# Optimization experiments

Hardware: AMD Instinct MI355X
Metric: run time of the kernel (lower is better)

Reference implementation:

```python
import jax, jax.numpy as jnp
import numpy as np

B, C, H, Wd = 4, 64, 64, 64


def setup_inputs() -> dict:
    key = jax.random.key(0)
    k1, k2, k3 = jax.random.split(key, 3)
    x = jax.random.normal(k1, (B, C, H, Wd), dtype=jnp.float32)
    W = jax.random.normal(k2, (C, C), dtype=jnp.float32) * (1.0 / np.sqrt(C))
    b = jax.random.normal(k3, (C,), dtype=jnp.float32) * 0.01
    return {"x": x, "W": W, "b": b}


def reference(x, W, b):
    Bz, Cz, Hz, Wz = x.shape
    N = Hz * Wz
    xf = x.reshape(Bz, Cz, N)                      # values [B,C,N]
    # shared 1x1 conv for queries and keys (same module instance in torch)
    qk = jnp.einsum('oc,bcn->bon', W, xf) + b[None, :, None]  # [B,C,N]
    # scores[b,n,m] = sum_c q[b,c,n] * k[b,c,m], scaled by 1/N
    scores = jnp.einsum('bcn,bcm->bnm', qk, qk) / N           # [B,N,N]
    attn = jax.nn.softmax(scores, axis=-1)                    # softmax over m
    # out[b,c,n] = sum_m values[b,c,m] * attn[b,n,m]
    out = jnp.einsum('bcm,bnm->bcn', xf, attn)
    return out.reshape(Bz, Cz, Hz, Wz)
```

## Files before the change

### kernel.cpp

```cpp
#include <hip/hip_runtime.h>
#include <hip/hip_bf16.h>

#define BATCH 4
#define NSP   4096

#define QKSCALE 0.0187675376f

typedef __bf16 bf16x8v __attribute__((ext_vector_type(8)));
typedef __bf16 bf16x4v __attribute__((ext_vector_type(4)));
typedef float  floatx4 __attribute__((ext_vector_type(4)));
typedef float  floatx16 __attribute__((ext_vector_type(16)));
typedef unsigned uivec2 __attribute__((ext_vector_type(2)));

static __device__ __forceinline__ float fast_exp2(float x) {
#if __has_builtin(__builtin_amdgcn_exp2f)
    return __builtin_amdgcn_exp2f(x);
#else
    return exp2f(x);
#endif
}

static __device__ __forceinline__ unsigned pkbf(float a, float b) {
    union { __bf16 h[2]; unsigned u; } x;
    x.h[0] = (__bf16)a; x.h[1] = (__bf16)b;
    return x.u;
}

static __device__ __forceinline__ void plswap(unsigned &a, unsigned &b) {
#if __has_builtin(__builtin_amdgcn_permlane32_swap)
    uivec2 r = __builtin_amdgcn_permlane32_swap(a, b, false, false);
    a = r[0]; b = r[1];
#else
    asm("v_permlane32_swap_b32 %0, %1" : "+v"(a), "+v"(b));
#endif
}

__global__ __launch_bounds__(256) void qk_kernel(const float* __restrict__ x,
                                                 const float* __restrict__ Wm,
                                                 const float* __restrict__ bias,
                                                 __bf16* __restrict__ qkT,
                                                 __bf16* __restrict__ xbf) {
    __shared__ __align__(16) __bf16 xT[64 * 72];

    const int t  = threadIdx.x;
    const int b  = blockIdx.x >> 6;
    const int n0 = (blockIdx.x & 63) << 6;

#pragma unroll
    for (int p = 0; p < 4; ++p) {
        const int c  = p * 16 + (t >> 4);
        const int n4 = (t & 15) * 4;
        const float4 v = *(const float4*)(x + (size_t)(b * 64 + c) * 4096 + n0 + n4);
        xT[(n4 + 0) * 72 + c] = (__bf16)(v.x * QKSCALE);
        xT[(n4 + 1) * 72 + c] = (__bf16)(v.y * QKSCALE);
        xT[(n4 + 2) * 72 + c] = (__bf16)(v.z * QKSCALE);
        xT[(n4 + 3) * 72 + c] = (__bf16)(v.w * QKSCALE);
        bf16x4v xv;
        xv[0] = (__bf16)v.x; xv[1] = (__bf16)v.y; xv[2] = (__bf16)v.z; xv[3] = (__bf16)v.w;
        *(bf16x4v*)(xbf + (size_t)(b * 64 + c) * 4096 + n0 + n4) = xv;
    }
    __syncthreads();

    const int w = t >> 6, lane = t & 63, quad = lane >> 4, l16 = lane & 15;
    const bf16x8v a0 = *(const bf16x8v*)(xT + (w * 16 + l16) * 72 + quad * 8);
    const bf16x8v a1 = *(const bf16x8v*)(xT + (w * 16 + l16) * 72 + 32 + quad * 8);

    floatx4 acc[4];
#pragma unroll
    for (int ot = 0; ot < 4; ++ot) {
        const float* wr = Wm + (ot * 16 + l16) * 64;
        float4 wa = *(const float4*)(wr + quad * 8);
        float4 wb = *(const float4*)(wr + quad * 8 + 4);
        float4 wc = *(const float4*)(wr + 32 + quad * 8);
        float4 wd = *(const float4*)(wr + 32 + quad * 8 + 4);
        bf16x8v b0, b1;
        b0[0]=(__bf16)wa.x; b0[1]=(__bf16)wa.y; b0[2]=(__bf16)wa.z; b0[3]=(__bf16)wa.w;
        b0[4]=(__bf16)wb.x; b0[5]=(__bf16)wb.y; b0[6]=(__bf16)wb.z; b0[7]=(__bf16)wb.w;
        b1[0]=(__bf16)wc.x; b1[1]=(__bf16)wc.y; b1[2]=(__bf16)wc.z; b1[3]=(__bf16)wc.w;
        b1[4]=(__bf16)wd.x; b1[5]=(__bf16)wd.y; b1[6]=(__bf16)wd.z; b1[7]=(__bf16)wd.w;
        acc[ot] = floatx4{0.f, 0.f, 0.f, 0.f};
        acc[ot] = __builtin_amdgcn_mfma_f32_16x16x32_bf16(a0, b0, acc[ot], 0, 0, 0);
        acc[ot] = __builtin_amdgcn_mfma_f32_16x16x32_bf16(a1, b1, acc[ot], 0, 0, 0);
    }
    __syncthreads();

#pragma unroll
    for (int ot = 0; ot < 4; ++ot) {
        const float bo = bias[ot * 16 + l16] * QKSCALE;
#pragma unroll
        for (int r = 0; r < 4; ++r)
            xT[(w * 16 + quad * 4 + r) * 72 + ot * 16 + l16] = (__bf16)(acc[ot][r] + bo);
    }
    __syncthreads();

    const int n = t >> 2, seg = t & 3;
    __bf16* dst = qkT + (size_t)(b * 4096 + n0 + n) * 64 + seg * 16;
    *(bf16x8v*)dst       = *(const bf16x8v*)(xT + n * 72 + seg * 16);
    *(bf16x8v*)(dst + 8) = *(const bf16x8v*)(xT + n * 72 + seg * 16 + 8);
}

template<int SPLIT, int ITERS>
__global__ __launch_bounds__(256, 2) void attn_kernel(const __bf16* __restrict__ xbf,
                                                      const __bf16* __restrict__ qkT,
                                                      __bf16* __restrict__ Opart,
                                                      float* __restrict__ Lpart) {
    __shared__ __align__(16) char smem[66560];
    __bf16* Klds = (__bf16*)smem;
    __bf16* Vlds = (__bf16*)(smem + 16384);
    float*  Olds = (float*)smem;

    const int t   = threadIdx.x;
    const int blk = blockIdx.x;
    const int xcd = blk & 7;
    const int b   = xcd >> 1;
    const int sub = ((blk >> 3) << 1) | (xcd & 1);
    const int qt  = sub / SPLIT;
    const int s   = sub % SPLIT;
    const int n0  = qt << 8;
    const int pblk = (b * 16 + qt) * SPLIT + s;

    const int w = t >> 6, lane = t & 63, l31 = lane & 31, hi = lane >> 5;

    const __bf16* kgl = qkT + (size_t)b * 4096 * 64;
    const __bf16* vgl = xbf + (size_t)b * 64 * 4096;

    bf16x8v qf[2][4];
#pragma unroll
    for (int qt2 = 0; qt2 < 2; ++qt2) {
        const __bf16* qrow = kgl + (size_t)(n0 + w * 64 + qt2 * 32 + l31) * 64;
#pragma unroll
        for (int kb = 0; kb < 4; ++kb)
            qf[qt2][kb] = *(const bf16x8v*)(qrow + kb * 16 + hi * 8);
    }

    floatx16 oacc[2][2] = {};
    float rs[2] = {0.f, 0.f};

    const int srow = t >> 3;
    const int scol = t & 7;
    const int slot = ((scol ^ (srow & 7)) * 8);
    uint4 kst0, kst1, vst0, vst1;
    auto stage_load = [&](int m0) {
        kst0 = *(const uint4*)(kgl + (size_t)(m0 + srow) * 64 + scol * 8);
        kst1 = *(const uint4*)(kgl + (size_t)(m0 + srow + 32) * 64 + scol * 8);
        vst0 = *(const uint4*)(vgl + (size_t)srow * 4096 + m0 + scol * 8);
        vst1 = *(const uint4*)(vgl + (size_t)(srow + 32) * 4096 + m0 + scol * 8);
    };
    auto stage_write = [&](int buf) {
        __bf16* kd = Klds + buf * 4096;
        __bf16* vd = Vlds + buf * 4096;
        *(uint4*)(kd + srow * 64 + slot)        = kst0;
        *(uint4*)(kd + (srow + 32) * 64 + slot) = kst1;
        *(uint4*)(vd + srow * 64 + slot)        = vst0;
        *(uint4*)(vd + (srow + 32) * 64 + slot) = vst1;
    };

    const int mbase = s * (64 * ITERS);
    stage_load(mbase);
    stage_write(0);
    int cur = 0;

    for (int it = 0; it < ITERS; ++it) {
        if (it + 1 < ITERS) stage_load(mbase + ((it + 1) << 6));
        __syncthreads();
        const __bf16* Kc = Klds + cur * 4096;
        const __bf16* Vc = Vlds + cur * 4096;

        __builtin_amdgcn_s_setprio(1);
#pragma unroll
        for (int mt = 0; mt < 2; ++mt) {
            bf16x8v kf[4];
#pragma unroll
            for (int kb = 0; kb < 4; ++kb)
                kf[kb] = *(const bf16x8v*)(Kc + (mt * 32 + l31) * 64 +
                                           (((kb * 2 + hi) ^ (l31 & 7)) * 8));

            bf16x8v vf[2][2];
#pragma unroll
            for (int ct = 0; ct < 2; ++ct)
#pragma unroll
                for (int ks = 0; ks < 2; ++ks)
                    vf[ct][ks] = *(const bf16x8v*)(Vc + (ct * 32 + l31) * 64 +
                                                   (((mt * 4 + ks * 2 + hi) ^ (l31 & 7)) * 8));

#pragma unroll
            for (int qt2 = 0; qt2 < 2; ++qt2) {
                floatx16 acc = {};
#pragma unroll
                for (int kb = 0; kb < 4; ++kb)
                    acc = __builtin_amdgcn_mfma_f32_32x32x16_bf16(kf[kb], qf[qt2][kb], acc, 0, 0, 0);

                float p[16];
                float sum = 0.f;
#pragma unroll
                for (int i = 0; i < 16; ++i) { p[i] = fast_exp2(acc[i]); sum += p[i]; }
                rs[qt2] += sum;

                unsigned wd0 = pkbf(p[0],  p[1]),  wd1 = pkbf(p[2],  p[3]);
                unsigned wd2 = pkbf(p[4],  p[5]),  wd3 = pkbf(p[6],  p[7]);
                unsigned wd4 = pkbf(p[8],  p[9]),  wd5 = pkbf(p[10], p[11]);
                unsigned wd6 = pkbf(p[12], p[13]), wd7 = pkbf(p[14], p[15]);
                plswap(wd0, wd2);
                plswap(wd1, wd3);
                plswap(wd4, wd6);
                plswap(wd5, wd7);
                union { unsigned u[4]; bf16x8v v; } pb0, pb1;
                pb0.u[0] = wd0; pb0.u[1] = wd1; pb0.u[2] = wd2; pb0.u[3] = wd3;
                pb1.u[0] = wd4; pb1.u[1] = wd5; pb1.u[2] = wd6; pb1.u[3] = wd7;

#pragma unroll
                for (int ct = 0; ct < 2; ++ct) {
                    oacc[qt2][ct] = __builtin_amdgcn_mfma_f32_32x32x16_bf16(vf[ct][0], pb0.v, oacc[qt2][ct], 0, 0, 0);
                    oacc[qt2][ct] = __builtin_amdgcn_mfma_f32_32x32x16_bf16(vf[ct][1], pb1.v, oacc[qt2][ct], 0, 0, 0);
                }
            }
        }
        __builtin_amdgcn_s_setprio(0);

        if (it + 1 < ITERS) stage_write(cur ^ 1);
        cur ^= 1;
    }

#pragma unroll
    for (int qt2 = 0; qt2 < 2; ++qt2) {
        float v = rs[qt2] + __shfl_xor(rs[qt2], 32, 64);
        if (lane < 32)
            Lpart[(size_t)pblk * 256 + w * 64 + qt2 * 32 + l31] = v;
    }

    __syncthreads();

#pragma unroll
    for (int qt2 = 0; qt2 < 2; ++qt2)
#pragma unroll
        for (int ct = 0; ct < 2; ++ct)
#pragma unroll
            for (int r = 0; r < 16; ++r) {
                const int c = ct * 32 + (r & 3) + 8 * (r >> 2) + 4 * hi;
                Olds[c * 260 + w * 64 + qt2 * 32 + l31] = oacc[qt2][ct][r];
            }
    __syncthreads();

    const int c = t >> 2, qb = (t & 3) * 64;
#pragma unroll
    for (int i = 0; i < 8; ++i) {
        floatx4 v0 = *(const floatx4*)(Olds + c * 260 + qb + i * 8);
        floatx4 v1 = *(const floatx4*)(Olds + c * 260 + qb + i * 8 + 4);
        bf16x8v pk;
        pk[0]=(__bf16)v0[0]; pk[1]=(__bf16)v0[1]; pk[2]=(__bf16)v0[2]; pk[3]=(__bf16)v0[3];
        pk[4]=(__bf16)v1[0]; pk[5]=(__bf16)v1[1]; pk[6]=(__bf16)v1[2]; pk[7]=(__bf16)v1[3];
        *(bf16x8v*)(Opart + (size_t)pblk * 16384 + c * 256 + qb + i * 8) = pk;
    }
}

template<int SPLIT>
__global__ __launch_bounds__(256) void reduce_kernel(const __bf16* __restrict__ Opart,
                                                     const float* __restrict__ Lpart,
                                                     float* __restrict__ out) {
    const int blk = blockIdx.x;
    const int bq = blk >> 3, cq = blk & 7;
    const int b = bq >> 4, qt = bq & 15;
    const int t = threadIdx.x;
    const int c  = cq * 8 + (t >> 5);
    const int q8 = (t & 31) * 8;

    float l[8] = {0.f,0.f,0.f,0.f,0.f,0.f,0.f,0.f};
#pragma unroll
    for (int s = 0; s < SPLIT; ++s) {
        const float* lp = Lpart + ((size_t)bq * SPLIT + s) * 256 + q8;
        float4 u = *(const float4*)lp;
        float4 v = *(const float4*)(lp + 4);
        l[0]+=u.x; l[1]+=u.y; l[2]+=u.z; l[3]+=u.w;
        l[4]+=v.x; l[5]+=v.y; l[6]+=v.z; l[7]+=v.w;
    }
    float a[8] = {0.f,0.f,0.f,0.f,0.f,0.f,0.f,0.f};
#pragma unroll
    for (int s = 0; s < SPLIT; ++s) {
        bf16x8v v = *(const bf16x8v*)(Opart + ((size_t)bq * SPLIT + s) * 16384 + c * 256 + q8);
#pragma unroll
        for (int k = 0; k < 8; ++k) a[k] += (float)v[k];
    }
    float* op = out + (size_t)(b * 64 + c) * 4096 + qt * 256 + q8;
    float4 o0, o1;
    o0.x = a[0]/l[0]; o0.y = a[1]/l[1]; o0.z = a[2]/l[2]; o0.w = a[3]/l[3];
    o1.x = a[4]/l[4]; o1.y = a[5]/l[5]; o1.z = a[6]/l[6]; o1.w = a[7]/l[7];
    *(float4*)op       = o0;
    *(float4*)(op + 4) = o1;
}

extern "C" void kernel_launch(void* const* d_in, const int* in_sizes, int n_in,
                              void* d_out, int out_size, void* d_ws, size_t ws_size,
                              hipStream_t stream) {
    const float* x    = (const float*)d_in[0];
    const float* Wm   = (const float*)d_in[1];
    const float* bias = (const float*)d_in[2];
    float* out = (float*)d_out;

    char* ws = (char*)d_ws;
    __bf16* qkT = (__bf16*)ws;
    __bf16* xbf = (__bf16*)(ws + 2097152);

    qk_kernel<<<BATCH * (NSP / 64), 256, 0, stream>>>(x, Wm, bias, qkT, xbf);

    const size_t HEAD = 2097152 + 2097152;
    const size_t needBig = HEAD + (size_t)512 * 16384 * 2 + (size_t)512 * 256 * 4;
    if (ws_size >= needBig) {
        __bf16* Opart = (__bf16*)(ws + HEAD);
        float*  Lpart = (float*)(ws + HEAD + (size_t)512 * 16384 * 2);
        attn_kernel<8, 8><<<BATCH * 16 * 8, 256, 0, stream>>>(xbf, qkT, Opart, Lpart);
        reduce_kernel<8><<<512, 256, 0, stream>>>(Opart, Lpart, out);
    } else {
        __bf16* Opart = (__bf16*)(ws + HEAD);
        float*  Lpart = (float*)(ws + HEAD + (size_t)256 * 16384 * 2);
        attn_kernel<4, 16><<<BATCH * 16 * 4, 256, 0, stream>>>(xbf, qkT, Opart, Lpart);
        reduce_kernel<4><<<512, 256, 0, stream>>>(Opart, Lpart, out);
    }
}
```

Baseline: 98.37 us.

## Use 8 waves per attention block with one 32-query tile per wave

Result: faster. 96.33 us (-2.1%).

```diff
diff --git a/kernel.cpp b/kernel.cpp
--- a/kernel.cpp
+++ b/kernel.cpp
@@ -100,7 +100,7 @@
 }
 
 template<int SPLIT, int ITERS>
-__global__ __launch_bounds__(256, 2) void attn_kernel(const __bf16* __restrict__ xbf,
+__global__ __launch_bounds__(512, 4) void attn_kernel(const __bf16* __restrict__ xbf,
                                                       const __bf16* __restrict__ qkT,
                                                       __bf16* __restrict__ Opart,
                                                       float* __restrict__ Lpart) {
@@ -124,35 +124,28 @@
     const __bf16* kgl = qkT + (size_t)b * 4096 * 64;
     const __bf16* vgl = xbf + (size_t)b * 64 * 4096;
 
-    bf16x8v qf[2][4];
-#pragma unroll
-    for (int qt2 = 0; qt2 < 2; ++qt2) {
-        const __bf16* qrow = kgl + (size_t)(n0 + w * 64 + qt2 * 32 + l31) * 64;
+    bf16x8v qf[4];
+    {
+        const __bf16* qrow = kgl + (size_t)(n0 + w * 32 + l31) * 64;
 #pragma unroll
         for (int kb = 0; kb < 4; ++kb)
-            qf[qt2][kb] = *(const bf16x8v*)(qrow + kb * 16 + hi * 8);
-    }
-
-    floatx16 oacc[2][2] = {};
-    float rs[2] = {0.f, 0.f};
+            qf[kb] = *(const bf16x8v*)(qrow + kb * 16 + hi * 8);
+    }
+
+    floatx16 oacc[2] = {};
+    float rs = 0.f;
 
     const int srow = t >> 3;
     const int scol = t & 7;
     const int slot = ((scol ^ (srow & 7)) * 8);
-    uint4 kst0, kst1, vst0, vst1;
+    uint4 kst, vst;
     auto stage_load = [&](int m0) {
-        kst0 = *(const uint4*)(kgl + (size_t)(m0 + srow) * 64 + scol * 8);
-        kst1 = *(const uint4*)(kgl + (size_t)(m0 + srow + 32) * 64 + scol * 8);
-        vst0 = *(const uint4*)(vgl + (size_t)srow * 4096 + m0 + scol * 8);
-        vst1 = *(const uint4*)(vgl + (size_t)(srow + 32) * 4096 + m0 + scol * 8);
+        kst = *(const uint4*)(kgl + (size_t)(m0 + srow) * 64 + scol * 8);
+        vst = *(const uint4*)(vgl + (size_t)srow * 4096 + m0 + scol * 8);
     };
     auto stage_write = [&](int buf) {
-        __bf16* kd = Klds + buf * 4096;
-        __bf16* vd = Vlds + buf * 4096;
-        *(uint4*)(kd + srow * 64 + slot)        = kst0;
-        *(uint4*)(kd + (srow + 32) * 64 + slot) = kst1;
-        *(uint4*)(vd + srow * 64 + slot)        = vst0;
-        *(uint4*)(vd + (srow + 32) * 64 + slot) = vst1;
+        *(uint4*)(Klds + buf * 4096 + srow * 64 + slot) = kst;
+        *(uint4*)(Vlds + buf * 4096 + srow * 64 + slot) = vst;
     };
 
     const int mbase = s * (64 * ITERS);
@@ -183,36 +176,33 @@
                     vf[ct][ks] = *(const bf16x8v*)(Vc + (ct * 32 + l31) * 64 +
                                                    (((mt * 4 + ks * 2 + hi) ^ (l31 & 7)) * 8));
 
-#pragma unroll
-            for (int qt2 = 0; qt2 < 2; ++qt2) {
-                floatx16 acc = {};
-#pragma unroll
-                for (int kb = 0; kb < 4; ++kb)
-                    acc = __builtin_amdgcn_mfma_f32_32x32x16_bf16(kf[kb], qf[qt2][kb], acc, 0, 0, 0);
-
-                float p[16];
-                float sum = 0.f;
-#pragma unroll
-                for (int i = 0; i < 16; ++i) { p[i] = fast_exp2(acc[i]); sum += p[i]; }
-                rs[qt2] += sum;
-
-                unsigned wd0 = pkbf(p[0],  p[1]),  wd1 = pkbf(p[2],  p[3]);
-                unsigned wd2 = pkbf(p[4],  p[5]),  wd3 = pkbf(p[6],  p[7]);
-                unsigned wd4 = pkbf(p[8],  p[9]),  wd5 = pkbf(p[10], p[11]);
-                unsigned wd6 = pkbf(p[12], p[13]), wd7 = pkbf(p[14], p[15]);
-                plswap(wd0, wd2);
-                plswap(wd1, wd3);
-                plswap(wd4, wd6);
-                plswap(wd5, wd7);
-                union { unsigned u[4]; bf16x8v v; } pb0, pb1;
-                pb0.u[0] = wd0; pb0.u[1] = wd1; pb0.u[2] = wd2; pb0.u[3] = wd3;
-                pb1.u[0] = wd4; pb1.u[1] = wd5; pb1.u[2] = wd6; pb1.u[3] = wd7;
-
-#pragma unroll
-                for (int ct = 0; ct < 2; ++ct) {
-                    oacc[qt2][ct] = __builtin_amdgcn_mfma_f32_32x32x16_bf16(vf[ct][0], pb0.v, oacc[qt2][ct], 0, 0, 0);
-                    oacc[qt2][ct] = __builtin_amdgcn_mfma_f32_32x32x16_bf16(vf[ct][1], pb1.v, oacc[qt2][ct], 0, 0, 0);
-                }
+            floatx16 acc = {};
+#pragma unroll
+            for (int kb = 0; kb < 4; ++kb)
+                acc = __builtin_amdgcn_mfma_f32_32x32x16_bf16(kf[kb], qf[kb], acc, 0, 0, 0);
+
+            float p[16];
+            float sum = 0.f;
+#pragma unroll
+            for (int i = 0; i < 16; ++i) { p[i] = fast_exp2(acc[i]); sum += p[i]; }
+            rs += sum;
+
+            unsigned wd0 = pkbf(p[0],  p[1]),  wd1 = pkbf(p[2],  p[3]);
+            unsigned wd2 = pkbf(p[4],  p[5]),  wd3 = pkbf(p[6],  p[7]);
+            unsigned wd4 = pkbf(p[8],  p[9]),  wd5 = pkbf(p[10], p[11]);
+            unsigned wd6 = pkbf(p[12], p[13]), wd7 = pkbf(p[14], p[15]);
+            plswap(wd0, wd2);
+            plswap(wd1, wd3);
+            plswap(wd4, wd6);
+            plswap(wd5, wd7);
+            union { unsigned u[4]; bf16x8v v; } pb0, pb1;
+            pb0.u[0] = wd0; pb0.u[1] = wd1; pb0.u[2] = wd2; pb0.u[3] = wd3;
+            pb1.u[0] = wd4; pb1.u[1] = wd5; pb1.u[2] = wd6; pb1.u[3] = wd7;
+
+#pragma unroll
+            for (int ct = 0; ct < 2; ++ct) {
+                oacc[ct] = __builtin_amdgcn_mfma_f32_32x32x16_bf16(vf[ct][0], pb0.v, oacc[ct], 0, 0, 0);
+                oacc[ct] = __builtin_amdgcn_mfma_f32_32x32x16_bf16(vf[ct][1], pb1.v, oacc[ct], 0, 0, 0);
             }
         }
         __builtin_amdgcn_s_setprio(0);
@@ -221,35 +211,32 @@
         cur ^= 1;
     }
 
-#pragma unroll
-    for (int qt2 = 0; qt2 < 2; ++qt2) {
-        float v = rs[qt2] + __shfl_xor(rs[qt2], 32, 64);
+    {
+        float v = rs + __shfl_xor(rs, 32, 64);
         if (lane < 32)
-            Lpart[(size_t)pblk * 256 + w * 64 + qt2 * 32 + l31] = v;
-    }
-
-    __syncthreads();
-
-#pragma unroll
-    for (int qt2 = 0; qt2 < 2; ++qt2)
-#pragma unroll
-        for (int ct = 0; ct < 2; ++ct)
-#pragma unroll
-            for (int r = 0; r < 16; ++r) {
-                const int c = ct * 32 + (r & 3) + 8 * (r >> 2) + 4 * hi;
-                Olds[c * 260 + w * 64 + qt2 * 32 + l31] = oacc[qt2][ct][r];
-            }
-    __syncthreads();
-
-    const int c = t >> 2, qb = (t & 3) * 64;
-#pragma unroll
-    for (int i = 0; i < 8; ++i) {
-        floatx4 v0 = *(const floatx4*)(Olds + c * 260 + qb + i * 8);
-        floatx4 v1 = *(const floatx4*)(Olds + c * 260 + qb + i * 8 + 4);
+            Lpart[(size_t)pblk * 256 + w * 32 + l31] = v;
+    }
+
+    __syncthreads();
+
+#pragma unroll
+    for (int ct = 0; ct < 2; ++ct)
+#pragma unroll
+        for (int r = 0; r < 16; ++r) {
+            const int c = ct * 32 + (r & 3) + 8 * (r >> 2) + 4 * hi;
+            Olds[c * 260 + w * 32 + l31] = oacc[ct][r];
+        }
+    __syncthreads();
+
+    const int c = t >> 3, qs = (t & 7) * 32;
+#pragma unroll
+    for (int i = 0; i < 4; ++i) {
+        floatx4 v0 = *(const floatx4*)(Olds + c * 260 + qs + i * 8);
+        floatx4 v1 = *(const floatx4*)(Olds + c * 260 + qs + i * 8 + 4);
         bf16x8v pk;
         pk[0]=(__bf16)v0[0]; pk[1]=(__bf16)v0[1]; pk[2]=(__bf16)v0[2]; pk[3]=(__bf16)v0[3];
         pk[4]=(__bf16)v1[0]; pk[5]=(__bf16)v1[1]; pk[6]=(__bf16)v1[2]; pk[7]=(__bf16)v1[3];
-        *(bf16x8v*)(Opart + (size_t)pblk * 16384 + c * 256 + qb + i * 8) = pk;
+        *(bf16x8v*)(Opart + (size_t)pblk * 16384 + c * 256 + qs + i * 8) = pk;
     }
 }
 
@@ -307,12 +294,12 @@
     if (ws_size >= needBig) {
         __bf16* Opart = (__bf16*)(ws + HEAD);
         float*  Lpart = (float*)(ws + HEAD + (size_t)512 * 16384 * 2);
-        attn_kernel<8, 8><<<BATCH * 16 * 8, 256, 0, stream>>>(xbf, qkT, Opart, Lpart);
+        attn_kernel<8, 8><<<BATCH * 16 * 8, 512, 0, stream>>>(xbf, qkT, Opart, Lpart);
         reduce_kernel<8><<<512, 256, 0, stream>>>(Opart, Lpart, out);
     } else {
         __bf16* Opart = (__bf16*)(ws + HEAD);
         float*  Lpart = (float*)(ws + HEAD + (size_t)256 * 16384 * 2);
-        attn_kernel<4, 16><<<BATCH * 16 * 4, 256, 0, stream>>>(xbf, qkT, Opart, Lpart);
+        attn_kernel<4, 16><<<BATCH * 16 * 4, 512, 0, stream>>>(xbf, qkT, Opart, Lpart);
         reduce_kernel<4><<<512, 256, 0, stream>>>(Opart, Lpart, out);
     }
 }
```
